# Kernel optimization log

Measured on AMD Instinct MI355X. Metric: run time of the kernel, lower is better.

## Reference

```python
import jax, jax.numpy as jnp
import numpy as np
import math
from jax.scipy.special import logsumexp

B, S, D, H, L, FF, T, V = 32, 512, 512, 8, 2, 2048, 32, 32000
DH = D // H
LN_EPS = 1e-5
NEG = -1e9


def make_pe(seq_len, d_model):
    pos = np.arange(seq_len, dtype=np.float32)[:, None]
    div = np.exp(np.arange(0, d_model, 2, dtype=np.float32) * (-np.log(10000.0) / d_model))
    pe = np.zeros((seq_len, d_model), np.float32)
    pe[:, 0::2] = np.sin(pos * div)
    pe[:, 1::2] = np.cos(pos * div)
    return jnp.asarray(pe)


def layer_norm(x, scale, bias):
    mu = x.mean(-1, keepdims=True)
    var = ((x - mu) ** 2).mean(-1, keepdims=True)
    return (x - mu) / jnp.sqrt(var + LN_EPS) * scale + bias


def setup_inputs() -> dict:
    key = jax.random.key(0)
    ks = jax.random.split(key, 16)
    w = lambda k, shape, s=0.02: (jax.random.normal(k, shape, dtype=jnp.float32) * s)
    inp = {
        'tokens': jax.random.randint(ks[0], (B, S), 0, V),
        'tags': jax.random.randint(ks[1], (B, S), 0, T),
        'mask': jnp.ones((B, S), dtype=bool),
        'emb': w(ks[2], (V, D)),
        'Wqkv': w(ks[3], (L, 3 * D, D)),
        'bqkv': jnp.zeros((L, 3 * D), jnp.float32),
        'Wo': w(ks[4], (L, D, D)),
        'bo': jnp.zeros((L, D), jnp.float32),
        'ln1_s': jnp.ones((L, D), jnp.float32),
        'ln1_b': jnp.zeros((L, D), jnp.float32),
        'W1': w(ks[5], (L, FF, D)),
        'b1': jnp.zeros((L, FF), jnp.float32),
        'W2': w(ks[6], (L, D, FF)),
        'b2': jnp.zeros((L, D), jnp.float32),
        'ln2_s': jnp.ones((L, D), jnp.float32),
        'ln2_b': jnp.zeros((L, D), jnp.float32),
        'Wtag': w(ks[7], (T, D)),
        'btag': jnp.zeros((T,), jnp.float32),
        'trans': w(ks[8], (T, T), 0.1),
        'start_t': w(ks[9], (T,), 0.1),
        'end_t': w(ks[10], (T,), 0.1),
    }
    return inp


def _forward(tokens, tags, mask, emb, Wqkv, bqkv, Wo, bo, ln1_s, ln1_b, W1, b1, W2, b2,
             ln2_s, ln2_b, Wtag, btag, trans, start_t, end_t):
    # --- embedding + positional encoding ---
    x = emb[tokens] + make_pe(S, D)[None]  # [B,S,D]
    # --- transformer encoder (post-norm, relu, batch_first) ---
    for l in range(L):
        qkv = x @ Wqkv[l].T + bqkv[l]
        q, k, v = jnp.split(qkv, 3, axis=-1)
        q = q.reshape(B, S, H, DH).transpose(0, 2, 1, 3)
        k = k.reshape(B, S, H, DH).transpose(0, 2, 1, 3)
        v = v.reshape(B, S, H, DH).transpose(0, 2, 1, 3)
        scores = jnp.einsum('bhqd,bhkd->bhqk', q, k) / math.sqrt(DH)
        scores = jnp.where(mask[:, None, None, :], scores, NEG)  # key padding mask
        attn = jax.nn.softmax(scores, axis=-1)
        o = jnp.einsum('bhqk,bhkd->bhqd', attn, v).transpose(0, 2, 1, 3).reshape(B, S, D)
        x = layer_norm(x + o @ Wo[l].T + bo[l], ln1_s[l], ln1_b[l])
        h = jax.nn.relu(x @ W1[l].T + b1[l])
        x = layer_norm(x + h @ W2[l].T + b2[l], ln2_s[l], ln2_b[l])
    emissions = x @ Wtag.T + btag  # [B,S,T]

    maskf = mask.astype(emissions.dtype)
    # --- gold path score ---
    emit_sel = jnp.take_along_axis(emissions, tags[..., None], axis=2)[..., 0]  # [B,S]
    trans_sel = trans[tags[:, :-1], tags[:, 1:]]  # [B,S-1]
    score = start_t[tags[:, 0]] + emit_sel[:, 0]
    score = score + jnp.sum((trans_sel + emit_sel[:, 1:]) * maskf[:, 1:], axis=1)
    last_pos = mask.astype(jnp.int32).sum(axis=1) - 1
    last_tags = jnp.take_along_axis(tags, last_pos[:, None], axis=1)[:, 0]
    score = score + end_t[last_tags]

    # --- log partition: forward algorithm as a scan over time ---
    alpha0 = start_t[None] + emissions[:, 0]  # [B,T]

    def step(alpha, inp):
        emit_t, m_t = inp  # [B,T], [B]
        new = logsumexp(alpha[:, :, None] + trans[None] + emit_t[:, None, :], axis=1)
        alpha = jnp.where(m_t[:, None], new, alpha)
        return alpha, None

    alpha, _ = jax.lax.scan(step, alpha0,
                            (emissions[:, 1:].transpose(1, 0, 2), mask[:, 1:].T))
    log_z = logsumexp(alpha + end_t[None], axis=1)
    return (log_z - score).mean()


def reference(tokens, tags, mask, emb, Wqkv, bqkv, Wo, bo, ln1_s, ln1_b, W1, b1, W2, b2,
              ln2_s, ln2_b, Wtag, btag, trans, start_t, end_t):
    return _forward(tokens, tags, mask, emb, Wqkv, bqkv, Wo, bo, ln1_s, ln1_b, W1, b1,
                    W2, b2, ln2_s, ln2_b, Wtag, btag, trans, start_t, end_t)
```

## Files before the change

### kernel.cpp

```cpp
#include <hip/hip_runtime.h>

#define Bz 32
#define Sz 512
#define Dz 512
#define Hz 8
#define Lz 2
#define FFz 2048
#define Tz 32
#define DHz 64

typedef unsigned short u16;
typedef __attribute__((ext_vector_type(8))) short short8;
typedef __attribute__((ext_vector_type(4))) short short4v;
typedef __attribute__((ext_vector_type(4))) float f32x4;

__device__ __forceinline__ float b2f(u16 s) {
    union { unsigned u; float f; } x; x.u = ((unsigned)s) << 16; return x.f;
}
__device__ __forceinline__ u16 f2b(float f) {
    union { float f; unsigned u; } x; x.f = f;
    unsigned r = x.u + 0x7FFFu + ((x.u >> 16) & 1u);
    return (u16)(r >> 16);
}

__device__ __forceinline__ void gload_lds16(const void* g, void* l) {
    __builtin_amdgcn_global_load_lds((const __attribute__((address_space(1))) void*)g,
                                     (__attribute__((address_space(3))) void*)l, 16, 0, 0);
}

template<int BM, int BN, bool OUT_BF16, bool RELU>
__global__ __launch_bounds__(256) void gemm_k(
    const u16* __restrict__ A, int lda, long sAb, long sAh,
    const u16* __restrict__ Bm, int ldb, long sBb, long sBh,
    void* __restrict__ Cm, int ldc, long sCb, long sCh,
    const float* __restrict__ bias,
    const u16* __restrict__ res, int ldres,
    float scale, int K, int nh)
{
    constexpr int WM = BM / 2, WN = BN / 2;
    constexpr int TM = WM / 16, TN = WN / 16;
    __shared__ __align__(16) u16 ldsA[BM * 64];
    __shared__ __align__(16) u16 ldsB[BN * 64];

    const int tid = threadIdx.x, lane = tid & 63, w = tid >> 6;
    const int wm = w >> 1, wn = w & 1;
    const int z = blockIdx.z, zb = z / nh, zh = z % nh;
    A  += (size_t)zb * sAb + (size_t)zh * sAh;
    Bm += (size_t)zb * sBb + (size_t)zh * sBh;
    char* Cc = (char*)Cm + ((size_t)zb * sCb + (size_t)zh * sCh) * (OUT_BF16 ? 2 : 4);

    const int m0 = blockIdx.y * BM, n0 = blockIdx.x * BN;
    f32x4 acc[TM][TN];
#pragma unroll
    for (int mi = 0; mi < TM; ++mi)
#pragma unroll
        for (int ni = 0; ni < TN; ++ni) acc[mi][ni] = (f32x4){0.f, 0.f, 0.f, 0.f};

    const int sr = lane >> 3;
    const int scsw = (((lane & 7) ^ sr) << 3);

    for (int k0 = 0; k0 < K; k0 += 64) {
        const int ra = w * (BM / 4);
#pragma unroll
        for (int t = 0; t < BM / 32; ++t) {
            const u16* g = A + (size_t)(m0 + ra + t * 8 + sr) * lda + k0 + scsw;
            gload_lds16(g, &ldsA[(ra + t * 8) * 64]);
        }
        const int rb = w * (BN / 4);
#pragma unroll
        for (int t = 0; t < BN / 32; ++t) {
            const u16* g = Bm + (size_t)(n0 + rb + t * 8 + sr) * ldb + k0 + scsw;
            gload_lds16(g, &ldsB[(rb + t * 8) * 64]);
        }
        asm volatile("s_waitcnt vmcnt(0)" ::: "memory");
        __syncthreads();
#pragma unroll
        for (int kk = 0; kk < 64; kk += 32) {
            const int kc = (kk >> 3) + (lane >> 4);
            const int sw = ((kc ^ (lane & 7)) << 3);
            short8 af[TM], bf[TN];
#pragma unroll
            for (int mi = 0; mi < TM; ++mi)
                af[mi] = *(const short8*)&ldsA[(wm * WM + mi * 16 + (lane & 15)) * 64 + sw];
#pragma unroll
            for (int ni = 0; ni < TN; ++ni)
                bf[ni] = *(const short8*)&ldsB[(wn * WN + ni * 16 + (lane & 15)) * 64 + sw];
#pragma unroll
            for (int mi = 0; mi < TM; ++mi)
#pragma unroll
                for (int ni = 0; ni < TN; ++ni)
                    acc[mi][ni] = __builtin_amdgcn_mfma_f32_16x16x32_bf16(bf[ni], af[mi], acc[mi][ni], 0, 0, 0);
        }
        __syncthreads();
    }
#pragma unroll
    for (int mi = 0; mi < TM; ++mi) {
        const int m = m0 + wm * WM + mi * 16 + (lane & 15);
#pragma unroll
        for (int ni = 0; ni < TN; ++ni) {
            const int n = n0 + wn * WN + ni * 16 + ((lane >> 4) << 2);
            float v0 = acc[mi][ni][0] * scale, v1 = acc[mi][ni][1] * scale;
            float v2 = acc[mi][ni][2] * scale, v3 = acc[mi][ni][3] * scale;
            if (bias) {
                const float4 b4 = *(const float4*)&bias[n];
                v0 += b4.x; v1 += b4.y; v2 += b4.z; v3 += b4.w;
            }
            if (res) {
                const short4v r4 = *(const short4v*)&res[(size_t)m * ldres + n];
                v0 += b2f((u16)r4[0]); v1 += b2f((u16)r4[1]);
                v2 += b2f((u16)r4[2]); v3 += b2f((u16)r4[3]);
            }
            if (RELU) {
                v0 = fmaxf(v0, 0.f); v1 = fmaxf(v1, 0.f);
                v2 = fmaxf(v2, 0.f); v3 = fmaxf(v3, 0.f);
            }
            if (OUT_BF16) {
                short4v pk;
                pk[0] = (short)f2b(v0); pk[1] = (short)f2b(v1);
                pk[2] = (short)f2b(v2); pk[3] = (short)f2b(v3);
                *(short4v*)&((u16*)Cc)[(size_t)m * ldc + n] = pk;
            } else {
                f32x4 o = (f32x4){v0, v1, v2, v3};
                *(f32x4*)&((float*)Cc)[(size_t)m * ldc + n] = o;
            }
        }
    }
}

__global__ __launch_bounds__(256, 3) void attn_k(const u16* __restrict__ qkv,
                                                 const u16* __restrict__ vt,
                                                 u16* __restrict__ ao)
{
    __shared__ __align__(16) char smem[34816];
    __shared__ float ldsM[2][2][64], ldsL[2][2][64];
    const int tid = threadIdx.x, lane = tid & 63, w = tid >> 6;
    const int wkv = w >> 1, wqm = w & 1;
    const int z = blockIdx.x, qt = blockIdx.y;
    const int bb = z >> 3, hh = z & 7;
    const int quad = lane >> 4, c = lane & 15;

    u16* myP = (u16*)smem + w * (64 * 40);
    float* ldsO = (float*)smem;

    const u16* qbase = qkv + (size_t)(bb * Sz + qt * 128 + wqm * 64) * 1536 + hh * 64;
    short8 qf[4][2];
#pragma unroll
    for (int ni = 0; ni < 4; ++ni)
#pragma unroll
        for (int kk = 0; kk < 2; ++kk)
            qf[ni][kk] = *(const short8*)(qbase + (size_t)(ni * 16 + c) * 1536 + kk * 32 + quad * 8);

    f32x4 oacc[4][4];
    float mst[4], lst[4];
#pragma unroll
    for (int i = 0; i < 4; ++i) {
        mst[i] = -1e30f; lst[i] = 0.f;
#pragma unroll
        for (int j2 = 0; j2 < 4; ++j2) oacc[i][j2] = (f32x4){0.f, 0.f, 0.f, 0.f};
    }

    const u16* kbase = qkv + (size_t)(bb * Sz) * 1536 + 512 + hh * 64;
    const u16* vbase = vt + (size_t)z * (64 * 512);

#pragma unroll 2
    for (int jt = 0; jt < 8; ++jt) {
        const int kv0 = wkv * 256 + jt * 32;
        short8 kf[2][2];
#pragma unroll
        for (int mi = 0; mi < 2; ++mi)
#pragma unroll
            for (int kk = 0; kk < 2; ++kk)
                kf[mi][kk] = *(const short8*)(kbase + (size_t)(kv0 + mi * 16 + c) * 1536 + kk * 32 + quad * 8);
        f32x4 sacc[2][4];
#pragma unroll
        for (int mi = 0; mi < 2; ++mi)
#pragma unroll
            for (int ni = 0; ni < 4; ++ni) sacc[mi][ni] = (f32x4){0.f, 0.f, 0.f, 0.f};
#pragma unroll
        for (int kk = 0; kk < 2; ++kk)
#pragma unroll
            for (int mi = 0; mi < 2; ++mi)
#pragma unroll
                for (int ni = 0; ni < 4; ++ni)
                    sacc[mi][ni] = __builtin_amdgcn_mfma_f32_16x16x32_bf16(kf[mi][kk], qf[ni][kk], sacc[mi][ni], 0, 0, 0);
        float mnew[4], alpha[4], lad[4];
#pragma unroll
        for (int ni = 0; ni < 4; ++ni) {
            float v = -1e30f;
#pragma unroll
            for (int mi = 0; mi < 2; ++mi)
#pragma unroll
                for (int r = 0; r < 4; ++r) v = fmaxf(v, sacc[mi][ni][r]);
            v *= 0.125f;
            v = fmaxf(v, __shfl_xor(v, 16));
            v = fmaxf(v, __shfl_xor(v, 32));
            mnew[ni] = fmaxf(mst[ni], v);
            alpha[ni] = __expf(mst[ni] - mnew[ni]);
            mst[ni] = mnew[ni];
            lad[ni] = 0.f;
        }
#pragma unroll
        for (int mi = 0; mi < 2; ++mi)
#pragma unroll
            for (int ni = 0; ni < 4; ++ni) {
                float p0 = __expf(sacc[mi][ni][0] * 0.125f - mnew[ni]);
                float p1 = __expf(sacc[mi][ni][1] * 0.125f - mnew[ni]);
                float p2 = __expf(sacc[mi][ni][2] * 0.125f - mnew[ni]);
                float p3 = __expf(sacc[mi][ni][3] * 0.125f - mnew[ni]);
                lad[ni] += (p0 + p1) + (p2 + p3);
                short4v pk;
                pk[0] = (short)f2b(p0); pk[1] = (short)f2b(p1);
                pk[2] = (short)f2b(p2); pk[3] = (short)f2b(p3);
                *(short4v*)&myP[(ni * 16 + c) * 40 + mi * 16 + quad * 4] = pk;
            }
#pragma unroll
        for (int ni = 0; ni < 4; ++ni) {
            float v = lad[ni];
            v += __shfl_xor(v, 16);
            v += __shfl_xor(v, 32);
            lst[ni] = lst[ni] * alpha[ni] + v;
        }
#pragma unroll
        for (int mi2 = 0; mi2 < 4; ++mi2)
#pragma unroll
            for (int ni = 0; ni < 4; ++ni) {
                oacc[mi2][ni][0] *= alpha[ni]; oacc[mi2][ni][1] *= alpha[ni];
                oacc[mi2][ni][2] *= alpha[ni]; oacc[mi2][ni][3] *= alpha[ni];
            }
        short8 vf[4], pf[4];
#pragma unroll
        for (int mi2 = 0; mi2 < 4; ++mi2)
            vf[mi2] = *(const short8*)(vbase + (size_t)(mi2 * 16 + c) * 512 + kv0 + quad * 8);
#pragma unroll
        for (int ni = 0; ni < 4; ++ni)
            pf[ni] = *(const short8*)&myP[(ni * 16 + c) * 40 + quad * 8];
#pragma unroll
        for (int mi2 = 0; mi2 < 4; ++mi2)
#pragma unroll
            for (int ni = 0; ni < 4; ++ni)
                oacc[mi2][ni] = __builtin_amdgcn_mfma_f32_16x16x32_bf16(vf[mi2], pf[ni], oacc[mi2][ni], 0, 0, 0);
    }
    if (quad == 0) {
#pragma unroll
        for (int ni = 0; ni < 4; ++ni) {
            ldsM[wkv][wqm][ni * 16 + c] = mst[ni];
            ldsL[wkv][wqm][ni * 16 + c] = lst[ni];
        }
    }
    __syncthreads();
    float wmy[4], Linv[4];
#pragma unroll
    for (int ni = 0; ni < 4; ++ni) {
        float m0 = ldsM[0][wqm][ni * 16 + c], m1 = ldsM[1][wqm][ni * 16 + c];
        float M = fmaxf(m0, m1);
        float L = ldsL[0][wqm][ni * 16 + c] * __expf(m0 - M) + ldsL[1][wqm][ni * 16 + c] * __expf(m1 - M);
        wmy[ni] = __expf(mst[ni] - M);
        Linv[ni] = 1.f / L;
    }
    __syncthreads();
    if (wkv == 1) {
#pragma unroll
        for (int mi2 = 0; mi2 < 4; ++mi2)
#pragma unroll
            for (int ni = 0; ni < 4; ++ni) {
                f32x4 o = oacc[mi2][ni];
                o[0] *= wmy[ni]; o[1] *= wmy[ni]; o[2] *= wmy[ni]; o[3] *= wmy[ni];
                *(f32x4*)&ldsO[((size_t)wqm * 64 + ni * 16 + c) * 68 + mi2 * 16 + quad * 4] = o;
            }
    }
    __syncthreads();
    if (wkv == 0) {
#pragma unroll
        for (int mi2 = 0; mi2 < 4; ++mi2)
#pragma unroll
            for (int ni = 0; ni < 4; ++ni) {
                f32x4 oth = *(const f32x4*)&ldsO[((size_t)wqm * 64 + ni * 16 + c) * 68 + mi2 * 16 + quad * 4];
                int m = qt * 128 + wqm * 64 + ni * 16 + c;
                short4v pk;
#pragma unroll
                for (int r = 0; r < 4; ++r)
                    pk[r] = (short)f2b((oacc[mi2][ni][r] * wmy[ni] + oth[r]) * Linv[ni]);
                *(short4v*)&ao[(size_t)(bb * Sz + m) * 512 + hh * 64 + mi2 * 16 + quad * 4] = pk;
            }
    }
}

__global__ __launch_bounds__(256) void prep_k(
    const float* __restrict__ Wqkv, const float* __restrict__ Wo,
    const float* __restrict__ W1, const float* __restrict__ W2,
    const float* __restrict__ wt, const float* __restrict__ bt,
    u16* __restrict__ wqkvb, u16* __restrict__ wob, u16* __restrict__ w1b,
    u16* __restrict__ w2b, u16* __restrict__ wtp, float* __restrict__ btp)
{
    const long n1 = (long)2 * 1536 * 512;
    const long n2 = n1 + (long)2 * 512 * 512;
    const long n3 = n2 + (long)2 * 2048 * 512;
    const long n4 = n3 + (long)2 * 512 * 2048;
    const long n5 = n4 + (long)64 * 512;
    long i = (long)blockIdx.x * 256 + threadIdx.x;
    if (i < n1) wqkvb[i] = f2b(Wqkv[i]);
    else if (i < n2) { long j = i - n1; wob[j] = f2b(Wo[j]); }
    else if (i < n3) { long j = i - n2; w1b[j] = f2b(W1[j]); }
    else if (i < n4) { long j = i - n3; w2b[j] = f2b(W2[j]); }
    else if (i < n5) { long j = i - n4; wtp[j] = ((j >> 9) < Tz) ? f2b(wt[j]) : (u16)0; }
    else if (i < n5 + 64) { long j = i - n5; btp[j] = (j < Tz) ? bt[j] : 0.f; }
}

__global__ __launch_bounds__(256) void embed_k(const int* __restrict__ tokens, const float* __restrict__ emb,
                                               u16* __restrict__ xb) {
    int bs = blockIdx.x * 4 + (threadIdx.x >> 6);
    int lane = threadIdx.x & 63;
    int s = bs & (Sz - 1);
    int tok = tokens[bs];
    const float* er = emb + (size_t)tok * Dz + lane * 8;
    float4 e0 = *(const float4*)er, e1 = *(const float4*)(er + 4);
    float e[8] = {e0.x, e0.y, e0.z, e0.w, e1.x, e1.y, e1.z, e1.w};
    short8 ov;
#pragma unroll
    for (int q = 0; q < 8; ++q) {
        int d = lane * 8 + q;
        int i2 = d & ~1;
        float div = expf(-(float)i2 * (9.210340371976184f / (float)Dz));
        float arg = (float)s * div;
        float pe = (d & 1) ? cosf(arg) : sinf(arg);
        ov[q] = (short)f2b(e[q] + pe);
    }
    *(short8*)&xb[(size_t)bs * Dz + lane * 8] = ov;
}

__global__ __launch_bounds__(256) void ln_k(const float* __restrict__ y, const float* __restrict__ sc,
                                            const float* __restrict__ bi, u16* __restrict__ xb) {
    int row = blockIdx.x * 4 + (threadIdx.x >> 6);
    int lane = threadIdx.x & 63;
    const float* yr = y + (size_t)row * Dz + lane * 8;
    float4 a = *(const float4*)yr, b = *(const float4*)(yr + 4);
    float v[8] = {a.x, a.y, a.z, a.w, b.x, b.y, b.z, b.w};
    float sum = 0.f, sq = 0.f;
#pragma unroll
    for (int q = 0; q < 8; ++q) { sum += v[q]; sq += v[q] * v[q]; }
    for (int o = 32; o; o >>= 1) { sum += __shfl_xor(sum, o); sq += __shfl_xor(sq, o); }
    float mu = sum * (1.f / Dz);
    float var = sq * (1.f / Dz) - mu * mu;
    float rstd = rsqrtf(var + 1e-5f);
    float4 s0 = *(const float4*)&sc[lane * 8], s1 = *(const float4*)&sc[lane * 8 + 4];
    float4 b0 = *(const float4*)&bi[lane * 8], b1 = *(const float4*)&bi[lane * 8 + 4];
    float scv[8] = {s0.x, s0.y, s0.z, s0.w, s1.x, s1.y, s1.z, s1.w};
    float biv[8] = {b0.x, b0.y, b0.z, b0.w, b1.x, b1.y, b1.z, b1.w};
    short8 ov;
#pragma unroll
    for (int q = 0; q < 8; ++q)
        ov[q] = (short)f2b((v[q] - mu) * rstd * scv[q] + biv[q]);
    *(short8*)&xb[(size_t)row * Dz + lane * 8] = ov;
}

__global__ __launch_bounds__(256) void transpose_v_k(const u16* __restrict__ qkv, u16* __restrict__ vt) {
    __shared__ u16 tile[64][72];
    int z = blockIdx.y; int bb = z >> 3, hh = z & 7;
    int s0 = blockIdx.x * 64;
    int t = threadIdx.x;
#pragma unroll
    for (int it = 0; it < 2; ++it) {
        int idx = it * 256 + t;
        int sl = idx >> 3, dv = idx & 7;
        const u16* g = qkv + (size_t)(bb * Sz + s0 + sl) * (3 * Dz) + 2 * Dz + hh * 64 + dv * 8;
        short8 vv = *(const short8*)g;
#pragma unroll
        for (int j = 0; j < 8; ++j) tile[sl][dv * 8 + j] = (u16)vv[j];
    }
    __syncthreads();
#pragma unroll
    for (int it = 0; it < 2; ++it) {
        int idx = it * 256 + t;
        int dh = idx >> 3, sv = idx & 7;
        short8 ov;
#pragma unroll
        for (int j = 0; j < 8; ++j) ov[j] = (short)tile[sv * 8 + j][dh];
        *(short8*)&vt[(size_t)z * DHz * Sz + (size_t)dh * Sz + s0 + sv * 8] = ov;
    }
}

__global__ __launch_bounds__(1024) void crf_span_k(
    const float* __restrict__ emis, const float* __restrict__ trans,
    float* __restrict__ Pout, float* __restrict__ lsout)
{
    __shared__ float E[32 * 32];
    __shared__ float Pb[2][32 * 32];
    __shared__ float wmax[16];
    __shared__ float smax_s, rinv_s, lsum_s;
    const int b = blockIdx.y, s = blockIdx.x;
    const int t0 = 1 + 32 * s;
    const int tend = min(Sz - 1, t0 + 31);
    const int tid = threadIdx.x;
    const int i = tid >> 5, j = tid & 31;
    const int w = tid >> 6;
    const float* em = emis + (size_t)b * Sz * 128;

    E[tid] = __expf(trans[tid]);
    if (tid == 0) { smax_s = 1.f; rinv_s = 1.f; lsum_s = 0.f; }
    __syncthreads();

    float Ecol[32];
#pragma unroll
    for (int k = 0; k < 32; ++k) Ecol[k] = E[k * 32 + j];

    Pb[0][i * 32 + j] = E[i * 32 + j] * __expf(em[(size_t)t0 * 128 + j]);
    __syncthreads();

    int cur = 0;
    float enext = __expf(em[(size_t)(t0 + 1) * 128 + j]);
    for (int t = t0 + 1; t <= tend; ++t) {
        float e = enext;
        if (t < tend) enext = __expf(em[(size_t)(t + 1) * 128 + j]);
        const float* Pr = &Pb[cur][i * 32];
        float v = 0.f;
#pragma unroll
        for (int k = 0; k < 32; ++k) v += Pr[k] * Ecol[k];
        v *= e * rinv_s;
        Pb[1 - cur][i * 32 + j] = v;
        float m = v;
        for (int o = 32; o; o >>= 1) m = fmaxf(m, __shfl_xor(m, o));
        if ((tid & 63) == 0) wmax[w] = m;
        __syncthreads();
        if (tid == 0) {
            float bm = wmax[0];
#pragma unroll
            for (int q = 1; q < 16; ++q) bm = fmaxf(bm, wmax[q]);
            lsum_s += __logf(smax_s);
            smax_s = bm;
            rinv_s = 1.f / bm;
        }
        __syncthreads();
        cur ^= 1;
    }
    Pout[(((size_t)b * 16 + s) * 32 + i) * 32 + j] = Pb[cur][i * 32 + j];
    if (tid == 0) lsout[b * 16 + s] = lsum_s;
}

__global__ __launch_bounds__(64) void crf2_k(
    const float* __restrict__ emis, const int* __restrict__ tags,
    const float* __restrict__ trans, const float* __restrict__ start_t,
    const float* __restrict__ end_t, const float* __restrict__ Pspan,
    const float* __restrict__ lsspan, float* __restrict__ diff)
{
    const int b = blockIdx.x, lane = threadIdx.x;
    const int* tg = tags + b * Sz;
    const float* em = emis + (size_t)b * Sz * 128;
    float partial = 0.f;
    for (int t = 1 + lane; t < Sz; t += 64) {
        int tp = tg[t - 1], tc = tg[t];
        partial += trans[tp * Tz + tc] + em[(size_t)t * 128 + tc];
    }
    for (int o = 32; o; o >>= 1) partial += __shfl_xor(partial, o);
    float score = partial + start_t[tg[0]] + em[tg[0]] + end_t[tg[Sz - 1]];

    const int j = lane & 31, hb = lane & 32;
    float a0 = start_t[j] + em[j];
    float m0 = a0;
    for (int o = 16; o; o >>= 1) m0 = fmaxf(m0, __shfl_xor(m0, o));
    float a = __expf(a0 - m0);
    float ls = m0;

    const float* Pb_ = Pspan + (size_t)b * 16 * 1024;
    float Pc[32];
#pragma unroll
    for (int k = 0; k < 32; ++k) Pc[k] = Pb_[k * 32 + j];
    for (int s = 0; s < 16; ++s) {
        float Pn[32];
        if (s < 15) {
#pragma unroll
            for (int k = 0; k < 32; ++k) Pn[k] = Pb_[(s + 1) * 1024 + k * 32 + j];
        }
        float an = 0.f;
#pragma unroll
        for (int k = 0; k < 32; ++k) an += __shfl(a, hb + k) * Pc[k];
        float am = an;
        for (int o = 16; o; o >>= 1) am = fmaxf(am, __shfl_xor(am, o));
        a = an / am;
        ls += __logf(am) + lsspan[b * 16 + s];
#pragma unroll
        for (int k = 0; k < 32; ++k) Pc[k] = Pn[k];
    }
    float wv = a * __expf(end_t[j]);
    for (int o = 16; o; o >>= 1) wv += __shfl_xor(wv, o);
    float logz = ls + __logf(wv);
    if (lane == 0) diff[b] = logz - score;
}

__global__ __launch_bounds__(64) void reduce_k(const float* __restrict__ diff, float* __restrict__ out) {
    int lane = threadIdx.x;
    float v = (lane < Bz) ? diff[lane] : 0.f;
    for (int o = 32; o; o >>= 1) v += __shfl_xor(v, o);
    if (lane == 0) out[0] = v / (float)Bz;
}

__global__ void sentinel_k(float* out, float v) {
    if (threadIdx.x == 0) out[0] = v;
}

extern "C" void kernel_launch(void* const* d_in, const int* in_sizes, int n_in,
                              void* d_out, int out_size, void* d_ws, size_t ws_size,
                              hipStream_t stream) {
    const int*   tokens = (const int*)d_in[0];
    const int*   tags   = (const int*)d_in[1];
    const float* emb    = (const float*)d_in[3];
    const float* Wqkv   = (const float*)d_in[4];
    const float* bqkv   = (const float*)d_in[5];
    const float* Wo     = (const float*)d_in[6];
    const float* bo     = (const float*)d_in[7];
    const float* ln1s   = (const float*)d_in[8];
    const float* ln1b   = (const float*)d_in[9];
    const float* W1     = (const float*)d_in[10];
    const float* b1     = (const float*)d_in[11];
    const float* W2     = (const float*)d_in[12];
    const float* b2     = (const float*)d_in[13];
    const float* ln2s   = (const float*)d_in[14];
    const float* ln2b   = (const float*)d_in[15];
    const float* Wtag   = (const float*)d_in[16];
    const float* btag   = (const float*)d_in[17];
    const float* trans  = (const float*)d_in[18];
    const float* start_t= (const float*)d_in[19];
    const float* end_t  = (const float*)d_in[20];

    char* base = (char*)d_ws;
    size_t off = 0;
    auto alloc = [&](size_t bytes) -> void* {
        void* p = base + off;
        off += (bytes + 255) & ~(size_t)255;
        return p;
    };
    u16*   xb    = (u16*)  alloc((size_t)16384 * 512 * 2);
    u16*   qkv   = (u16*)  alloc((size_t)16384 * 1536 * 2);
    u16*   vt    = (u16*)  alloc((size_t)256 * 64 * 512 * 2);
    u16*   ao    = (u16*)  alloc((size_t)16384 * 512 * 2);
    u16*   wqkvb = (u16*)  alloc((size_t)2 * 1536 * 512 * 2);
    u16*   wob   = (u16*)  alloc((size_t)2 * 512 * 512 * 2);
    u16*   w1b   = (u16*)  alloc((size_t)2 * 2048 * 512 * 2);
    u16*   w2b   = (u16*)  alloc((size_t)2 * 512 * 2048 * 2);
    u16*   wtagb = (u16*)  alloc((size_t)64 * 512 * 2);
    float* btagp = (float*)alloc(256);
    float* diff  = (float*)alloc(256);
    u16*   scratch=(u16*)  alloc((size_t)16384 * 2048 * 2);
    float* y     = (float*)qkv;
    float* emis  = (float*)ao;
    float* Pspan = (float*)scratch;
    float* lsspan= (float*)(scratch + 1048576);

    if (off > ws_size) {
        sentinel_k<<<1, 64, 0, stream>>>((float*)d_out, (float)ws_size);
        return;
    }

    {
        long total = (long)2 * 1536 * 512 + (long)2 * 512 * 512 + (long)2 * 2048 * 512
                   + (long)2 * 512 * 2048 + (long)64 * 512 + 64;
        prep_k<<<(int)((total + 255) / 256), 256, 0, stream>>>(
            Wqkv, Wo, W1, W2, Wtag, btag, wqkvb, wob, w1b, w2b, wtagb, btagp);
    }
    embed_k<<<4096, 256, 0, stream>>>(tokens, emb, xb);

    for (int l = 0; l < Lz; ++l) {
        gemm_k<128, 128, true, false><<<dim3(12, 128, 1), 256, 0, stream>>>(
            xb, 512, 0, 0, wqkvb + (size_t)l * 1536 * 512, 512, 0, 0,
            qkv, 1536, 0, 0, bqkv + l * 1536, nullptr, 0, 1.f, 512, 1);
        transpose_v_k<<<dim3(8, 256), 256, 0, stream>>>(qkv, vt);
        attn_k<<<dim3(256, 4), 256, 0, stream>>>(qkv, vt, ao);
        gemm_k<128, 128, false, false><<<dim3(4, 128, 1), 256, 0, stream>>>(
            ao, 512, 0, 0, wob + (size_t)l * 512 * 512, 512, 0, 0,
            y, 512, 0, 0, bo + l * 512, xb, 512, 1.f, 512, 1);
        ln_k<<<4096, 256, 0, stream>>>(y, ln1s + l * 512, ln1b + l * 512, xb);
        gemm_k<128, 128, true, true><<<dim3(16, 128, 1), 256, 0, stream>>>(
            xb, 512, 0, 0, w1b + (size_t)l * 2048 * 512, 512, 0, 0,
            scratch, 2048, 0, 0, b1 + l * 2048, nullptr, 0, 1.f, 512, 1);
        gemm_k<128, 128, false, false><<<dim3(4, 128, 1), 256, 0, stream>>>(
            scratch, 2048, 0, 0, w2b + (size_t)l * 512 * 2048, 2048, 0, 0,
            y, 512, 0, 0, b2 + l * 512, xb, 512, 1.f, 2048, 1);
        ln_k<<<4096, 256, 0, stream>>>(y, ln2s + l * 512, ln2b + l * 512, xb);
    }
    gemm_k<128, 64, false, false><<<dim3(1, 128, 1), 256, 0, stream>>>(
        xb, 512, 0, 0, wtagb, 512, 0, 0,
        emis, 128, 0, 0, btagp, nullptr, 0, 1.f, 512, 1);
    crf_span_k<<<dim3(16, Bz), 1024, 0, stream>>>(emis, trans, Pspan, lsspan);
    crf2_k<<<Bz, 64, 0, stream>>>(emis, tags, trans, start_t, end_t, Pspan, lsspan, diff);
    reduce_k<<<1, 64, 0, stream>>>(diff, (float*)d_out);
}
```

Baseline: 886.6 us.

## Drop split-KV within attention block; each wave owns 32 queries over full sequence

Previously each attention block split its four waves into two key/value halves by two 64-query groups, then merged partial softmax states through shared memory with three block barriers. Now each wave processes 32 queries across all 512 keys, so the cross-wave merge, its barriers and most of the shared memory go away. The trade-off is that each wave reuses each K/V fragment across fewer queries, so global/L2 traffic for K and V per block rises while register and LDS pressure fall. The occupancy hint in launch bounds is also removed.

```diff
diff --git a/kernel.cpp b/kernel.cpp
--- a/kernel.cpp
+++ b/kernel.cpp
@@ -127,65 +127,60 @@
     }
 }
 
-__global__ __launch_bounds__(256, 3) void attn_k(const u16* __restrict__ qkv,
-                                                 const u16* __restrict__ vt,
-                                                 u16* __restrict__ ao)
+__global__ __launch_bounds__(256) void attn_k(const u16* __restrict__ qkv,
+                                              const u16* __restrict__ vt,
+                                              u16* __restrict__ ao)
 {
-    __shared__ __align__(16) char smem[34816];
-    __shared__ float ldsM[2][2][64], ldsL[2][2][64];
+    __shared__ __align__(16) u16 ldsP[4][32 * 40];
     const int tid = threadIdx.x, lane = tid & 63, w = tid >> 6;
-    const int wkv = w >> 1, wqm = w & 1;
     const int z = blockIdx.x, qt = blockIdx.y;
     const int bb = z >> 3, hh = z & 7;
     const int quad = lane >> 4, c = lane & 15;
-
-    u16* myP = (u16*)smem + w * (64 * 40);
-    float* ldsO = (float*)smem;
-
-    const u16* qbase = qkv + (size_t)(bb * Sz + qt * 128 + wqm * 64) * 1536 + hh * 64;
-    short8 qf[4][2];
-#pragma unroll
-    for (int ni = 0; ni < 4; ++ni)
+    u16* myP = ldsP[w];
+    const int q0 = qt * 128 + w * 32;
+
+    const u16* qbase = qkv + (size_t)(bb * Sz + q0) * 1536 + hh * 64;
+    short8 qf[2][2];
+#pragma unroll
+    for (int ni = 0; ni < 2; ++ni)
 #pragma unroll
         for (int kk = 0; kk < 2; ++kk)
             qf[ni][kk] = *(const short8*)(qbase + (size_t)(ni * 16 + c) * 1536 + kk * 32 + quad * 8);
 
-    f32x4 oacc[4][4];
-    float mst[4], lst[4];
-#pragma unroll
-    for (int i = 0; i < 4; ++i) {
-        mst[i] = -1e30f; lst[i] = 0.f;
-#pragma unroll
-        for (int j2 = 0; j2 < 4; ++j2) oacc[i][j2] = (f32x4){0.f, 0.f, 0.f, 0.f};
-    }
+    f32x4 oacc[4][2];
+    float mst[2] = {-1e30f, -1e30f}, lst[2] = {0.f, 0.f};
+#pragma unroll
+    for (int i = 0; i < 4; ++i)
+#pragma unroll
+        for (int j2 = 0; j2 < 2; ++j2) oacc[i][j2] = (f32x4){0.f, 0.f, 0.f, 0.f};
 
     const u16* kbase = qkv + (size_t)(bb * Sz) * 1536 + 512 + hh * 64;
     const u16* vbase = vt + (size_t)z * (64 * 512);
 
 #pragma unroll 2
-    for (int jt = 0; jt < 8; ++jt) {
-        const int kv0 = wkv * 256 + jt * 32;
+    for (int jt = 0; jt < 16; ++jt) {
+        const int kv0 = jt * 32;
         short8 kf[2][2];
 #pragma unroll
         for (int mi = 0; mi < 2; ++mi)
 #pragma unroll
             for (int kk = 0; kk < 2; ++kk)
                 kf[mi][kk] = *(const short8*)(kbase + (size_t)(kv0 + mi * 16 + c) * 1536 + kk * 32 + quad * 8);
-        f32x4 sacc[2][4];
+        f32x4 sacc[2][2];
 #pragma unroll
         for (int mi = 0; mi < 2; ++mi)
 #pragma unroll
-            for (int ni = 0; ni < 4; ++ni) sacc[mi][ni] = (f32x4){0.f, 0.f, 0.f, 0.f};
+            for (int ni = 0; ni < 2; ++ni) sacc[mi][ni] = (f32x4){0.f, 0.f, 0.f, 0.f};
 #pragma unroll
         for (int kk = 0; kk < 2; ++kk)
 #pragma unroll
             for (int mi = 0; mi < 2; ++mi)
 #pragma unroll
-                for (int ni = 0; ni < 4; ++ni)
+                for (int ni = 0; ni < 2; ++ni)
                     sacc[mi][ni] = __builtin_amdgcn_mfma_f32_16x16x32_bf16(kf[mi][kk], qf[ni][kk], sacc[mi][ni], 0, 0, 0);
-        float mnew[4], alpha[4], lad[4];
-#pragma unroll
-        for (int ni = 0; ni < 4; ++ni) {
+        float mnew[2], alpha[2], lad[2];
+#pragma unroll
+        for (int ni = 0; ni < 2; ++ni) {
             float v = -1e30f;
 #pragma unroll
             for (int mi = 0; mi < 2; ++mi)
@@ -202,7 +197,7 @@
 #pragma unroll
         for (int mi = 0; mi < 2; ++mi)
 #pragma unroll
-            for (int ni = 0; ni < 4; ++ni) {
+            for (int ni = 0; ni < 2; ++ni) {
                 float p0 = __expf(sacc[mi][ni][0] * 0.125f - mnew[ni]);
                 float p1 = __expf(sacc[mi][ni][1] * 0.125f - mnew[ni]);
                 float p2 = __expf(sacc[mi][ni][2] * 0.125f - mnew[ni]);
@@ -214,7 +209,7 @@
                 *(short4v*)&myP[(ni * 16 + c) * 40 + mi * 16 + quad * 4] = pk;
             }
 #pragma unroll
-        for (int ni = 0; ni < 4; ++ni) {
+        for (int ni = 0; ni < 2; ++ni) {
             float v = lad[ni];
             v += __shfl_xor(v, 16);
             v += __shfl_xor(v, 32);
@@ -223,66 +218,35 @@
 #pragma unroll
         for (int mi2 = 0; mi2 < 4; ++mi2)
 #pragma unroll
-            for (int ni = 0; ni < 4; ++ni) {
+            for (int ni = 0; ni < 2; ++ni) {
                 oacc[mi2][ni][0] *= alpha[ni]; oacc[mi2][ni][1] *= alpha[ni];
                 oacc[mi2][ni][2] *= alpha[ni]; oacc[mi2][ni][3] *= alpha[ni];
             }
-        short8 vf[4], pf[4];
+        short8 vf[4], pf[2];
 #pragma unroll
         for (int mi2 = 0; mi2 < 4; ++mi2)
             vf[mi2] = *(const short8*)(vbase + (size_t)(mi2 * 16 + c) * 512 + kv0 + quad * 8);
 #pragma unroll
-        for (int ni = 0; ni < 4; ++ni)
+        for (int ni = 0; ni < 2; ++ni)
             pf[ni] = *(const short8*)&myP[(ni * 16 + c) * 40 + quad * 8];
 #pragma unroll
         for (int mi2 = 0; mi2 < 4; ++mi2)
 #pragma unroll
-            for (int ni = 0; ni < 4; ++ni)
+            for (int ni = 0; ni < 2; ++ni)
                 oacc[mi2][ni] = __builtin_amdgcn_mfma_f32_16x16x32_bf16(vf[mi2], pf[ni], oacc[mi2][ni], 0, 0, 0);
     }
-    if (quad == 0) {
-#pragma unroll
-        for (int ni = 0; ni < 4; ++ni) {
-            ldsM[wkv][wqm][ni * 16 + c] = mst[ni];
-            ldsL[wkv][wqm][ni * 16 + c] = lst[ni];
-        }
-    }
-    __syncthreads();
-    float wmy[4], Linv[4];
-#pragma unroll
-    for (int ni = 0; ni < 4; ++ni) {
-        float m0 = ldsM[0][wqm][ni * 16 + c], m1 = ldsM[1][wqm][ni * 16 + c];
-        float M = fmaxf(m0, m1);
-        float L = ldsL[0][wqm][ni * 16 + c] * __expf(m0 - M) + ldsL[1][wqm][ni * 16 + c] * __expf(m1 - M);
-        wmy[ni] = __expf(mst[ni] - M);
-        Linv[ni] = 1.f / L;
-    }
-    __syncthreads();
-    if (wkv == 1) {
-#pragma unroll
-        for (int mi2 = 0; mi2 < 4; ++mi2)
-#pragma unroll
-            for (int ni = 0; ni < 4; ++ni) {
-                f32x4 o = oacc[mi2][ni];
-                o[0] *= wmy[ni]; o[1] *= wmy[ni]; o[2] *= wmy[ni]; o[3] *= wmy[ni];
-                *(f32x4*)&ldsO[((size_t)wqm * 64 + ni * 16 + c) * 68 + mi2 * 16 + quad * 4] = o;
-            }
-    }
-    __syncthreads();
-    if (wkv == 0) {
-#pragma unroll
-        for (int mi2 = 0; mi2 < 4; ++mi2)
-#pragma unroll
-            for (int ni = 0; ni < 4; ++ni) {
-                f32x4 oth = *(const f32x4*)&ldsO[((size_t)wqm * 64 + ni * 16 + c) * 68 + mi2 * 16 + quad * 4];
-                int m = qt * 128 + wqm * 64 + ni * 16 + c;
-                short4v pk;
-#pragma unroll
-                for (int r = 0; r < 4; ++r)
-                    pk[r] = (short)f2b((oacc[mi2][ni][r] * wmy[ni] + oth[r]) * Linv[ni]);
-                *(short4v*)&ao[(size_t)(bb * Sz + m) * 512 + hh * 64 + mi2 * 16 + quad * 4] = pk;
-            }
-    }
+    float Linv[2] = {1.f / lst[0], 1.f / lst[1]};
+#pragma unroll
+    for (int mi2 = 0; mi2 < 4; ++mi2)
+#pragma unroll
+        for (int ni = 0; ni < 2; ++ni) {
+            int q = q0 + ni * 16 + c;
+            short4v pk;
+#pragma unroll
+            for (int r = 0; r < 4; ++r)
+                pk[r] = (short)f2b(oacc[mi2][ni][r] * Linv[ni]);
+            *(short4v*)&ao[(size_t)(bb * Sz + q) * 512 + hh * 64 + mi2 * 16 + quad * 4] = pk;
+        }
 }
 
 __global__ __launch_bounds__(256) void prep_k(
```

Result: faster. 803.0 us (-9.4%).
